# Optimization experiments

Measured on AMD Instinct MI355X. Metric: run time of the kernel, lower is better.

Reference implementation:

```python
import jax, jax.numpy as jnp
import numpy as np

B, T, D, H = 32, 512, 1024, 16
HD = D // H  # 64


def setup_inputs() -> dict:
    key = jax.random.key(0)
    ks = jax.random.split(key, 12)
    s_in = 1.0 / np.sqrt(D)
    x = jax.random.normal(ks[0], (B, T, D), dtype=jnp.float32)
    Wi = jax.random.normal(ks[1], (D, D), dtype=jnp.float32) * s_in
    bi = jnp.zeros((D,), dtype=jnp.float32)
    Wk = jax.random.normal(ks[2], (H, D, HD), dtype=jnp.float32) * s_in
    bk = jnp.zeros((H, HD), dtype=jnp.float32)
    Wq = jax.random.normal(ks[3], (H, D, HD), dtype=jnp.float32) * s_in
    bq = jnp.zeros((H, HD), dtype=jnp.float32)
    Wv = jax.random.normal(ks[4], (H, D, HD), dtype=jnp.float32) * s_in
    bv = jnp.zeros((H, HD), dtype=jnp.float32)
    Wo = jax.random.normal(ks[5], (D, D), dtype=jnp.float32) * s_in
    bo = jnp.zeros((D,), dtype=jnp.float32)
    return {"x": x, "Wi": Wi, "bi": bi, "Wk": Wk, "bk": bk,
            "Wq": Wq, "bq": bq, "Wv": Wv, "bv": bv, "Wo": Wo, "bo": bo}


def reference(x, Wi, bi, Wk, bk, Wq, bq, Wv, bv, Wo, bo):
    # in_proj
    h = x @ Wi + bi  # [B,T,D]
    # per-head K/Q/V projections, vectorized over heads
    k = jnp.einsum('btd,hde->bhte', h, Wk) + bk[None, :, None, :]  # [B,H,T,HD]
    q = jnp.einsum('btd,hde->bhte', h, Wq) + bq[None, :, None, :]
    v = jnp.einsum('btd,hde->bhte', h, Wv) + bv[None, :, None, :]
    # NOTE: original computes wei = k @ q^T (keys as rows), masks with tril,
    # softmax over last axis (queries). Faithfully reproduced (no scaling).
    wei = jnp.einsum('bhtd,bhsd->bhts', k, q)  # [B,H,T,T]
    causal = jnp.tril(jnp.ones((T, T), dtype=bool))
    wei = jnp.where(causal, wei, -jnp.inf)
    wei = jax.nn.softmax(wei, axis=-1)
    # dropout: eval mode (identity)
    out = jnp.einsum('bhts,bhsd->bhtd', wei, v)  # [B,H,T,HD]
    out = out.transpose(0, 2, 1, 3).reshape(B, T, D)  # concat heads on last dim
    return out @ Wo + bo
```

## Files before the change

kernel.cpp:

```cpp
#include <hip/hip_runtime.h>
#include <hip/hip_bf16.h>
#include <stdint.h>

#define NTOK 16384

typedef _Float16 f16;
typedef f16   f16x8 __attribute__((ext_vector_type(8)));
typedef float f32x4 __attribute__((ext_vector_type(4)));

__device__ __forceinline__ float bf2f(ushort h){
  union { uint32_t u; float f; } v; v.u = ((uint32_t)h) << 16; return v.f;
}
__device__ __forceinline__ ushort f2bf(float f){
  union { float f; uint32_t u; } v; v.f = f;
  uint32_t u = v.u;
  return (ushort)((u + 0x7FFFu + ((u >> 16) & 1u)) >> 16);
}
__device__ __forceinline__ ushort f2h(float f){
  return __builtin_bit_cast(ushort, (f16)f);
}
__device__ __forceinline__ f16x8 ld16(const ushort* p){
  uint4 u = *(const uint4*)p;
  return __builtin_bit_cast(f16x8, u);
}
__device__ __forceinline__ float ldf(const void* p, size_t idx, int isf32){
  if (isf32) return ((const float*)p)[idx];
  return bf2f(((const ushort*)p)[idx]);
}

__device__ __forceinline__ void stage64(const ushort* g, uint strideEl,
                                        ushort* ldsbase, uint tid){
  uint w = tid >> 6;
  #pragma unroll
  for (int i = 0; i < 2; ++i){
    uint c = i*256u + tid;
    const ushort* gp = g + (size_t)(c >> 3)*strideEl + (c & 7u)*8u;
    ushort* lp = ldsbase + (size_t)(i*256u + w*64u)*8u;
    __builtin_amdgcn_global_load_lds((const __attribute__((address_space(1))) void*)gp,
        (__attribute__((address_space(3))) void*)lp, 16, 0, 0);
  }
}

__global__ __launch_bounds__(256) void kdetect(const uint* __restrict__ wi, int* __restrict__ flag){
  __shared__ int cnt;
  if (threadIdx.x == 0) cnt = 0;
  __syncthreads();
  uint w = wi[threadIdx.x];
  uint e = (w >> 7) & 0xFFu;
  if (e >= 100u && e <= 130u) atomicAdd(&cnt, 1);
  __syncthreads();
  if (threadIdx.x == 0) flag[0] = (cnt < 128) ? 1 : 0;
}

__global__ __launch_bounds__(256) void kbias(const void* bi, const void* bo,
                                             const void* bk, const void* bq, const void* bv,
                                             const int* __restrict__ flag,
                                             float* bi_f, float* bo_f, float* bqkv_f){
  int f = flag[0];
  uint id = blockIdx.x*256u + threadIdx.x;
  if (id < 1024u)       bi_f[id]         = ldf(bi, id, f);
  else if (id < 2048u)  bo_f[id - 1024u] = ldf(bo, id - 1024u, f);
  else {
    uint j = id - 2048u;
    uint sel = j >> 10, i = j & 1023u;
    const void* src = (sel == 0) ? bk : ((sel == 1) ? bq : bv);
    bqkv_f[j] = ldf(src, i, f);
  }
}

__global__ __launch_bounds__(256) void ktranspose(const void* __restrict__ in,
                                                  const int* __restrict__ flag,
                                                  ushort* __restrict__ out){
  __shared__ float tile[64][65];
  int f = flag[0];
  uint R0 = blockIdx.x*64u, C0 = blockIdx.y*64u, t = threadIdx.x;
  #pragma unroll
  for (int i = 0; i < 16; ++i){
    uint id = i*256u + t, r = id >> 6, c = id & 63u;
    tile[r][c] = ldf(in, (size_t)(R0 + r)*1024u + C0 + c, f);
  }
  __syncthreads();
  #pragma unroll
  for (int i = 0; i < 16; ++i){
    uint id = i*256u + t, r = id >> 6, c = id & 63u;
    out[(size_t)(C0 + r)*1024u + R0 + c] = f2h(tile[c][r]);
  }
}

__global__ __launch_bounds__(256) void kqkvpack(const void* Wk, const void* Wq, const void* Wv,
                                                const int* __restrict__ flag,
                                                ushort* __restrict__ WqkvT){
  __shared__ float tile[64][65];
  int f = flag[0];
  uint sh = blockIdx.x;
  uint sel = sh >> 4, h = sh & 15u;
  uint D0 = blockIdx.y*64u, t = threadIdx.x;
  const void* W = (sel == 0) ? Wk : ((sel == 1) ? Wq : Wv);
  #pragma unroll
  for (int i = 0; i < 16; ++i){
    uint id = i*256u + t, r = id >> 6, c = id & 63u;
    tile[r][c] = ldf(W, (size_t)h*65536u + (size_t)(D0 + r)*64u + c, f);
  }
  __syncthreads();
  #pragma unroll
  for (int i = 0; i < 16; ++i){
    uint id = i*256u + t, r = id >> 6, c = id & 63u;
    WqkvT[(size_t)(sel*1024u + h*64u + r)*1024u + D0 + c] = f2h(tile[c][r]);
  }
}

__global__ __launch_bounds__(256) void kcvt_x(const void* __restrict__ x,
                                              const int* __restrict__ flag,
                                              ushort* __restrict__ xh){
  int f = flag[0];
  size_t g = (size_t)(blockIdx.x*256u + threadIdx.x)*8u;
  ushort o[8];
  if (f){
    const float* xf = (const float*)x + g;
    #pragma unroll
    for (int i = 0; i < 8; ++i) o[i] = f2h(xf[i]);
  } else {
    const ushort* xb = (const ushort*)x + g;
    #pragma unroll
    for (int i = 0; i < 8; ++i) o[i] = f2h(bf2f(xb[i]));
  }
  *(uint4*)(xh + g) = *(uint4*)o;
}

template<int MODE>
__global__ __launch_bounds__(256, 3) void kgemm(const ushort* __restrict__ A, const ushort* __restrict__ Bt,
                                                const float* __restrict__ bias, void* __restrict__ Cv,
                                                ushort* __restrict__ Vt, const int* __restrict__ dtf,
                                                int M, int N, int K){
  __shared__ ushort sA[128*32];
  __shared__ ushort sB[128*32];
  uint tid = threadIdx.x, w = tid >> 6, lane = tid & 63u, quad = lane >> 4, l15 = lane & 15u;
  uint bm = blockIdx.x, bn = blockIdx.y;
  uint wm = w >> 1, wn = w & 1u;
  f32x4 acc[4][4] = {};

  for (int k0 = 0; k0 < K; k0 += 32){
    #pragma unroll
    for (int i = 0; i < 2; ++i){
      uint c   = (w*2u + i)*64u + lane;
      uint row = c >> 2, ko = (c & 3u)*8u;
      const ushort* gA = A  + (size_t)(bm*128u + row)*K + k0 + ko;
      const ushort* gB = Bt + (size_t)(bn*128u + row)*K + k0 + ko;
      __builtin_amdgcn_global_load_lds((const __attribute__((address_space(1))) void*)gA,
          (__attribute__((address_space(3))) void*)(sA + (w*2u + i)*512u), 16, 0, 0);
      __builtin_amdgcn_global_load_lds((const __attribute__((address_space(1))) void*)gB,
          (__attribute__((address_space(3))) void*)(sB + (w*2u + i)*512u), 16, 0, 0);
    }
    __syncthreads();
    f16x8 aF[4], bF[4];
    #pragma unroll
    for (int i = 0; i < 4; ++i) aF[i] = *(const f16x8*)(sA + (wm*64u + i*16u + l15)*32u + quad*8u);
    #pragma unroll
    for (int j = 0; j < 4; ++j) bF[j] = *(const f16x8*)(sB + (wn*64u + j*16u + l15)*32u + quad*8u);
    #pragma unroll
    for (int i = 0; i < 4; ++i)
      #pragma unroll
      for (int j = 0; j < 4; ++j)
        acc[i][j] = __builtin_amdgcn_mfma_f32_16x16x32_f16(aF[i], bF[j], acc[i][j], 0, 0, 0);
    __syncthreads();
  }
  int f32out = (MODE == 2) ? dtf[0] : 0;
  #pragma unroll
  for (int j = 0; j < 4; ++j){
    uint col = bn*128u + wn*64u + j*16u + l15;
    float bj = bias[col];
    #pragma unroll
    for (int i = 0; i < 4; ++i){
      uint row0 = bm*128u + wm*64u + i*16u + quad*4u;
      #pragma unroll
      for (int r = 0; r < 4; ++r){
        float val = acc[i][j][r] + bj;
        uint row = row0 + r;
        if (MODE == 0){
          ((ushort*)Cv)[(size_t)row*N + col] = f2h(val);
        } else if (MODE == 1){
          if (col < 2048u){
            ((ushort*)Cv)[(size_t)row*2048u + col] = f2h(val);
          } else {
            uint c2 = col - 2048u;
            Vt[(size_t)(((row >> 9)*16u + (c2 >> 6))*64u + (c2 & 63u))*512u + (row & 511u)] = f2h(val);
          }
        } else {
          if (f32out) ((float*)Cv)[(size_t)row*N + col] = val;
          else        ((ushort*)Cv)[(size_t)row*N + col] = f2bf(val);
        }
      }
    }
  }
}

__global__ __launch_bounds__(256, 4) void kattn(const ushort* __restrict__ kq,
                                                const ushort* __restrict__ Vt,
                                                ushort* __restrict__ Out){
  __shared__ ushort sQ[2][64*64];
  __shared__ ushort sV[2][64*64];
  __shared__ ushort pbuf[4][16][64];
  uint tid = threadIdx.x, w = tid >> 6, lane = tid & 63u, quad = lane >> 4, l15 = lane & 15u;
  uint bh = blockIdx.x, tt = blockIdx.y;
  uint b = bh >> 4, h = bh & 15u;
  uint t0 = tt*64u;
  const float L2E = 1.44269504088896340736f;
  const float MNEG = -1.0e30f;

  stage64(kq + (size_t)(b*512u + t0)*2048u + h*64u, 2048u, (ushort*)pbuf, tid);
  stage64(kq + (size_t)(b*512u)*2048u + 1024u + h*64u, 2048u, sQ[0], tid);
  stage64(Vt + (size_t)(bh*64u)*512u, 512u, sV[0], tid);
  __syncthreads();

  f16x8 aK[2];
  {
    const ushort* kp = (const ushort*)pbuf + (size_t)(w*16u + l15)*64u + quad*8u;
    aK[0] = ld16(kp);
    aK[1] = ld16(kp + 32);
  }
  float m[4], l[4];
  f32x4 oacc[4];
  #pragma unroll
  for (int r = 0; r < 4; ++r){ m[r] = MNEG; l[r] = 0.f; }
  #pragma unroll
  for (int je = 0; je < 4; ++je) oacc[je] = (f32x4){0.f, 0.f, 0.f, 0.f};

  for (uint st = 0; st <= tt; ++st){
    uint cur = st & 1u;
    if (st) __syncthreads();
    f32x4 sacc[4];
    #pragma unroll
    for (int j = 0; j < 4; ++j){
      const ushort* qp = sQ[cur] + (size_t)(j*16u + l15)*64u + quad*8u;
      f16x8 bq0 = ld16(qp);
      f16x8 bq1 = ld16(qp + 32);
      f32x4 s = (f32x4){0.f, 0.f, 0.f, 0.f};
      s = __builtin_amdgcn_mfma_f32_16x16x32_f16(aK[0], bq0, s, 0, 0, 0);
      s = __builtin_amdgcn_mfma_f32_16x16x32_f16(aK[1], bq1, s, 0, 0, 0);
      #pragma unroll
      for (int r = 0; r < 4; ++r) s[r] = fminf(fmaxf(s[r], MNEG), 1.0e30f);
      sacc[j] = s;
    }
    if (st == tt){
      #pragma unroll
      for (int j = 0; j < 4; ++j)
        #pragma unroll
        for (int r = 0; r < 4; ++r)
          if (j*16u + l15 > w*16u + quad*4u + (uint)r) sacc[j][r] = MNEG;
    }
    float alpha[4];
    #pragma unroll
    for (int r = 0; r < 4; ++r){
      float v = fmaxf(fmaxf(sacc[0][r], sacc[1][r]), fmaxf(sacc[2][r], sacc[3][r]));
      v = fmaxf(v, __shfl_xor(v, 1));
      v = fmaxf(v, __shfl_xor(v, 2));
      v = fmaxf(v, __shfl_xor(v, 4));
      v = fmaxf(v, __shfl_xor(v, 8));
      float mn = fmaxf(m[r], v);
      alpha[r] = exp2f((m[r] - mn)*L2E);
      m[r] = mn;
    }
    #pragma unroll
    for (int j = 0; j < 4; ++j)
      #pragma unroll
      for (int r = 0; r < 4; ++r)
        sacc[j][r] = exp2f((sacc[j][r] - m[r])*L2E);
    #pragma unroll
    for (int r = 0; r < 4; ++r){
      float s = sacc[0][r] + sacc[1][r] + sacc[2][r] + sacc[3][r];
      s += __shfl_xor(s, 1);
      s += __shfl_xor(s, 2);
      s += __shfl_xor(s, 4);
      s += __shfl_xor(s, 8);
      l[r] = l[r]*alpha[r] + s;
    }
    #pragma unroll
    for (int je = 0; je < 4; ++je)
      #pragma unroll
      for (int r = 0; r < 4; ++r)
        oacc[je][r] *= alpha[r];
    #pragma unroll
    for (int j = 0; j < 4; ++j)
      #pragma unroll
      for (int r = 0; r < 4; ++r)
        pbuf[w][quad*4u + r][j*16u + l15] = f2h(sacc[j][r]);
    __syncthreads();
    if (st < tt){
      uint s1 = (st + 1u)*64u;
      stage64(kq + (size_t)(b*512u + s1)*2048u + 1024u + h*64u, 2048u, sQ[1u - cur], tid);
      stage64(Vt + (size_t)(bh*64u)*512u + s1, 512u, sV[1u - cur], tid);
    }
    f16x8 aP0 = *(const f16x8*)&pbuf[w][l15][quad*8u];
    f16x8 aP1 = *(const f16x8*)&pbuf[w][l15][32u + quad*8u];
    #pragma unroll
    for (int je = 0; je < 4; ++je){
      const ushort* vp = sV[cur] + (size_t)(je*16u + l15)*64u + quad*8u;
      f16x8 bv0 = ld16(vp);
      f16x8 bv1 = ld16(vp + 32);
      oacc[je] = __builtin_amdgcn_mfma_f32_16x16x32_f16(aP0, bv0, oacc[je], 0, 0, 0);
      oacc[je] = __builtin_amdgcn_mfma_f32_16x16x32_f16(aP1, bv1, oacc[je], 0, 0, 0);
    }
  }
  float inv[4];
  #pragma unroll
  for (int r = 0; r < 4; ++r) inv[r] = 1.0f / l[r];
  #pragma unroll
  for (int je = 0; je < 4; ++je){
    uint e = h*64u + je*16u + l15;
    #pragma unroll
    for (int r = 0; r < 4; ++r){
      uint t = t0 + w*16u + quad*4u + (uint)r;
      Out[(size_t)(b*512u + t)*1024u + e] = f2h(oacc[je][r]*inv[r]);
    }
  }
}


extern "C" void kernel_launch(void* const* d_in, const int* in_sizes, int n_in,
                              void* d_out, int out_size, void* d_ws, size_t ws_size,
                              hipStream_t stream){
  const void* x  = d_in[0];
  const void* Wi = d_in[1];
  const void* bi = d_in[2];
  const void* Wk = d_in[3];
  const void* bk = d_in[4];
  const void* Wq = d_in[5];
  const void* bq = d_in[6];
  const void* Wv = d_in[7];
  const void* bv = d_in[8];
  const void* Wo = d_in[9];
  const void* bo = d_in[10];
  char* ws = (char*)d_ws;

  const size_t MB = 1u << 20;
  int*    flag   = (int*)ws;
  float*  bi_f   = (float*)(ws + 4096);
  float*  bo_f   = (float*)(ws + 8192);
  float*  bqkv_f = (float*)(ws + 12288);
  ushort* WiT    = (ushort*)(ws + 32768);
  ushort* WoT    = (ushort*)(ws + 32768 + 2*MB);
  ushort* WqkvT  = (ushort*)(ws + 32768 + 4*MB);
  ushort* xh     = (ushort*)(ws + 32768 + 10*MB);
  ushort* kq     = (ushort*)(ws + 32768 + 10*MB);
  ushort* hbuf   = (ushort*)(ws + 32768 + 74*MB);
  ushort* Vt     = (ushort*)(ws + 32768 + 106*MB);

  kdetect<<<dim3(1), dim3(256), 0, stream>>>((const uint*)Wi, flag);
  kbias<<<dim3(20), dim3(256), 0, stream>>>(bi, bo, bk, bq, bv, flag, bi_f, bo_f, bqkv_f);
  ktranspose<<<dim3(16, 16), dim3(256), 0, stream>>>(Wi, flag, WiT);
  ktranspose<<<dim3(16, 16), dim3(256), 0, stream>>>(Wo, flag, WoT);
  kqkvpack<<<dim3(48, 16), dim3(256), 0, stream>>>(Wk, Wq, Wv, flag, WqkvT);
  kcvt_x<<<dim3(8192), dim3(256), 0, stream>>>(x, flag, xh);

  kgemm<0><<<dim3(128, 8),  dim3(256), 0, stream>>>(xh,   WiT,   bi_f,   hbuf, nullptr, nullptr, NTOK, 1024, 1024);
  kgemm<1><<<dim3(128, 24), dim3(256), 0, stream>>>(hbuf, WqkvT, bqkv_f, kq,   Vt,      nullptr, NTOK, 3072, 1024);
  kattn<<<dim3(512, 8), dim3(256), 0, stream>>>(kq, Vt, hbuf);
  kgemm<2><<<dim3(128, 8),  dim3(256), 0, stream>>>(hbuf, WoT,   bo_f,   d_out, nullptr, flag,   NTOK, 1024, 1024);
}
```

Before: 522.0 us.

## Swizzle attention LDS tiles, prefetch earlier, drop P barrier, raise gemm occupancy

Applies an XOR swizzle to the Q, V, K and P tiles in the attention kernel's LDS, both in the global-to-LDS staging and in every read, to avoid bank conflicts on the 16-byte fragment loads. It also moves the next-tile prefetch to the top of each loop iteration so it overlaps with the QK and softmax work. The block-wide barrier between writing and reading P is removed, since each wave only uses its own P buffer. Separately, the GEMM launch bounds now ask for 4 blocks per SIMD instead of 3, which may force register spilling.

```diff
diff --git a/kernel.cpp b/kernel.cpp
--- a/kernel.cpp
+++ b/kernel.cpp
@@ -28,13 +28,19 @@
   return bf2f(((const ushort*)p)[idx]);
 }
 
+__device__ __forceinline__ const ushort* swz(const ushort* base, uint row, uint chunk){
+  return base + (size_t)row*64u + (size_t)((chunk ^ (row & 7u))*8u);
+}
+
 __device__ __forceinline__ void stage64(const ushort* g, uint strideEl,
                                         ushort* ldsbase, uint tid){
   uint w = tid >> 6;
   #pragma unroll
   for (int i = 0; i < 2; ++i){
-    uint c = i*256u + tid;
-    const ushort* gp = g + (size_t)(c >> 3)*strideEl + (c & 7u)*8u;
+    uint lc  = i*256u + tid;
+    uint row = lc >> 3, cp = lc & 7u;
+    uint c   = cp ^ (row & 7u);
+    const ushort* gp = g + (size_t)row*strideEl + c*8u;
     ushort* lp = ldsbase + (size_t)(i*256u + w*64u)*8u;
     __builtin_amdgcn_global_load_lds((const __attribute__((address_space(1))) void*)gp,
         (__attribute__((address_space(3))) void*)lp, 16, 0, 0);
@@ -128,7 +134,7 @@
 }
 
 template<int MODE>
-__global__ __launch_bounds__(256, 3) void kgemm(const ushort* __restrict__ A, const ushort* __restrict__ Bt,
+__global__ __launch_bounds__(256, 4) void kgemm(const ushort* __restrict__ A, const ushort* __restrict__ Bt,
                                                 const float* __restrict__ bias, void* __restrict__ Cv,
                                                 ushort* __restrict__ Vt, const int* __restrict__ dtf,
                                                 int M, int N, int K){
@@ -199,7 +205,7 @@
                                                 ushort* __restrict__ Out){
   __shared__ ushort sQ[2][64*64];
   __shared__ ushort sV[2][64*64];
-  __shared__ ushort pbuf[4][16][64];
+  __shared__ ushort pbuf[4][16*64];
   uint tid = threadIdx.x, w = tid >> 6, lane = tid & 63u, quad = lane >> 4, l15 = lane & 15u;
   uint bh = blockIdx.x, tt = blockIdx.y;
   uint b = bh >> 4, h = bh & 15u;
@@ -213,27 +219,31 @@
   __syncthreads();
 
   f16x8 aK[2];
-  {
-    const ushort* kp = (const ushort*)pbuf + (size_t)(w*16u + l15)*64u + quad*8u;
-    aK[0] = ld16(kp);
-    aK[1] = ld16(kp + 32);
-  }
+  aK[0] = ld16(swz((const ushort*)pbuf, w*16u + l15, quad));
+  aK[1] = ld16(swz((const ushort*)pbuf, w*16u + l15, 4u + quad));
+
   float m[4], l[4];
   f32x4 oacc[4];
   #pragma unroll
   for (int r = 0; r < 4; ++r){ m[r] = MNEG; l[r] = 0.f; }
   #pragma unroll
   for (int je = 0; je < 4; ++je) oacc[je] = (f32x4){0.f, 0.f, 0.f, 0.f};
+
+  ushort* pw = (ushort*)pbuf + w*1024u;
 
   for (uint st = 0; st <= tt; ++st){
     uint cur = st & 1u;
     if (st) __syncthreads();
+    if (st < tt){
+      uint s1 = (st + 1u)*64u;
+      stage64(kq + (size_t)(b*512u + s1)*2048u + 1024u + h*64u, 2048u, sQ[1u - cur], tid);
+      stage64(Vt + (size_t)(bh*64u)*512u + s1, 512u, sV[1u - cur], tid);
+    }
     f32x4 sacc[4];
     #pragma unroll
     for (int j = 0; j < 4; ++j){
-      const ushort* qp = sQ[cur] + (size_t)(j*16u + l15)*64u + quad*8u;
-      f16x8 bq0 = ld16(qp);
-      f16x8 bq1 = ld16(qp + 32);
+      f16x8 bq0 = ld16(swz(sQ[cur], j*16u + l15, quad));
+      f16x8 bq1 = ld16(swz(sQ[cur], j*16u + l15, 4u + quad));
       f32x4 s = (f32x4){0.f, 0.f, 0.f, 0.f};
       s = __builtin_amdgcn_mfma_f32_16x16x32_f16(aK[0], bq0, s, 0, 0, 0);
       s = __builtin_amdgcn_mfma_f32_16x16x32_f16(aK[1], bq1, s, 0, 0, 0);
@@ -282,21 +292,16 @@
     #pragma unroll
     for (int j = 0; j < 4; ++j)
       #pragma unroll
-      for (int r = 0; r < 4; ++r)
-        pbuf[w][quad*4u + r][j*16u + l15] = f2h(sacc[j][r]);
-    __syncthreads();
-    if (st < tt){
-      uint s1 = (st + 1u)*64u;
-      stage64(kq + (size_t)(b*512u + s1)*2048u + 1024u + h*64u, 2048u, sQ[1u - cur], tid);
-      stage64(Vt + (size_t)(bh*64u)*512u + s1, 512u, sV[1u - cur], tid);
-    }
-    f16x8 aP0 = *(const f16x8*)&pbuf[w][l15][quad*8u];
-    f16x8 aP1 = *(const f16x8*)&pbuf[w][l15][32u + quad*8u];
+      for (int r = 0; r < 4; ++r){
+        uint t = quad*4u + (uint)r;
+        pw[t*64u + (((j*2u + (l15 >> 3)) ^ (t & 7u))*8u) + (l15 & 7u)] = f2h(sacc[j][r]);
+      }
+    f16x8 aP0 = ld16(swz(pw, l15, quad));
+    f16x8 aP1 = ld16(swz(pw, l15, 4u + quad));
     #pragma unroll
     for (int je = 0; je < 4; ++je){
-      const ushort* vp = sV[cur] + (size_t)(je*16u + l15)*64u + quad*8u;
-      f16x8 bv0 = ld16(vp);
-      f16x8 bv1 = ld16(vp + 32);
+      f16x8 bv0 = ld16(swz(sV[cur], je*16u + l15, quad));
+      f16x8 bv1 = ld16(swz(sV[cur], je*16u + l15, 4u + quad));
       oacc[je] = __builtin_amdgcn_mfma_f32_16x16x32_f16(aP0, bv0, oacc[je], 0, 0, 0);
       oacc[je] = __builtin_amdgcn_mfma_f32_16x16x32_f16(aP1, bv1, oacc[je], 0, 0, 0);
     }
```

Result: faster. 498.8 us (-4.5%).
